# Kernel tuning notes

Hardware: AMD Instinct MI355X
Metric: run time of the kernel (lower is better)

Reference implementation:

```python
import jax, jax.numpy as jnp
import numpy as np


def setup_inputs() -> dict:
    key = jax.random.key(0)
    k0, k1, k2, k3 = jax.random.split(key, 4)
    B, S, D, F, E = 2, 2048, 1024, 4096, 8
    hidden_states = jax.random.normal(k0, (B, S, D), dtype=jnp.float32)
    Wr = jax.random.normal(k1, (E, D), dtype=jnp.float32) * 0.02   # router Linear weight [E, D]
    W1 = jax.random.normal(k2, (E, D, F), dtype=jnp.float32) * 0.02  # expert w1 (transposed torch layout)
    W2 = jax.random.normal(k3, (E, F, D), dtype=jnp.float32) * 0.02  # expert w2
    return {"hidden_states": hidden_states, "Wr": Wr, "W1": W1, "W2": W2, "top_k": 2}


def reference(hidden_states, Wr, W1, W2, top_k):
    # hidden_states: [B, S, D]; Wr: [E, D]; W1: [E, D, F]; W2: [E, F, D]
    E = Wr.shape[0]
    dt = hidden_states.dtype

    # Router: logits -> top-k expert indices. NOTE: the original module computes
    # softmax routing weights over the top-k logits but never applies them in the
    # combine step, so the output is an UNWEIGHTED sum over selected experts.
    router_logits = jnp.einsum('bsd,ed->bse', hidden_states, Wr)
    _, topk_idx = jax.lax.top_k(router_logits, top_k)            # [B, S, K]

    # mask[b,s,e] = 1 if expert e is in token (b,s)'s top-k (indices are distinct)
    mask = (jax.nn.one_hot(topk_idx, E, dtype=dt).sum(axis=-2) > 0).astype(dt)  # [B, S, E]

    # Dense per-expert FFN (SiLU MLP, no bias, dropout=identity in eval):
    h = jax.nn.silu(jnp.einsum('bsd,edf->bsef', hidden_states, W1))  # [B, S, E, F]
    y = jnp.einsum('bsef,efd->bsed', h, W2)                          # [B, S, E, D]

    # Combine: unweighted sum over selected experts (faithful to source)
    return jnp.einsum('bsed,bse->bsd', y, mask)
```

## Files before the change

kernel.cpp:

```cpp
#include <hip/hip_runtime.h>
#include <hip/hip_bf16.h>
#include <stdint.h>

#define TOKENS 4096
#define DDIM 1024
#define FDIM 4096
#define NEXP 8
#define BM 128
#define BN 128
#define BK2 32

typedef __attribute__((ext_vector_type(4))) float f32x4;
typedef __attribute__((ext_vector_type(8))) short short8;

__device__ __forceinline__ unsigned short f2bf(float f) {
    union { float f; uint32_t u; } v; v.f = f;
    uint32_t u = v.u;
    return (unsigned short)((u + 0x7fff + ((u >> 16) & 1)) >> 16);
}

#define BARRIER() asm volatile("s_barrier" ::: "memory")
#define WAIT_VM0() asm volatile("s_waitcnt vmcnt(0)" ::: "memory")
#define WAIT_VM4() asm volatile("s_waitcnt vmcnt(4)" ::: "memory")
#define WAIT_VM8() asm volatile("s_waitcnt vmcnt(8)" ::: "memory")
#define WAIT_LGKM0() asm volatile("s_waitcnt lgkmcnt(0)" ::: "memory")
#define GLDS(SRC, DST) __builtin_amdgcn_global_load_lds( \
    (const __attribute__((address_space(1))) void*)(SRC), \
    (__attribute__((address_space(3))) void*)(DST), 16, 0, 0)

__device__ __forceinline__ short8 dsr(uint32_t addr) {
    short8 d;
    asm volatile("ds_read_b128 %0, %1" : "=v"(d) : "v"(addr));
    return d;
}

__global__ __launch_bounds__(256) void cvt_x(const float* __restrict__ x,
                                             unsigned short* __restrict__ xb, int n) {
    int i = (blockIdx.x * 256 + threadIdx.x) * 8;
    if (i >= n) return;
    float4 a = *(const float4*)(x + i);
    float4 b = *(const float4*)(x + i + 4);
    short8 o;
    o[0] = f2bf(a.x); o[1] = f2bf(a.y); o[2] = f2bf(a.z); o[3] = f2bf(a.w);
    o[4] = f2bf(b.x); o[5] = f2bf(b.y); o[6] = f2bf(b.z); o[7] = f2bf(b.w);
    *(short8*)(xb + i) = o;
}

__global__ __launch_bounds__(256) void transpose_cvt(const float* __restrict__ in,
                                                     unsigned short* __restrict__ out,
                                                     int R, int C) {
    __shared__ float tile[32][33];
    int e = blockIdx.z;
    int r0 = blockIdx.y * 32, c0 = blockIdx.x * 32;
    const float* src = in + (size_t)e * R * C;
    unsigned short* dst = out + (size_t)e * R * C;
    int t = threadIdx.x;
    int rr = t >> 3;
    int cc = (t & 7) * 4;
    float4 v = *(const float4*)(src + (size_t)(r0 + rr) * C + c0 + cc);
    tile[rr][cc + 0] = v.x; tile[rr][cc + 1] = v.y;
    tile[rr][cc + 2] = v.z; tile[rr][cc + 3] = v.w;
    __syncthreads();
    int oc = rr;
    int orr = cc;
    ushort4 o;
    o.x = f2bf(tile[orr + 0][oc]);
    o.y = f2bf(tile[orr + 1][oc]);
    o.z = f2bf(tile[orr + 2][oc]);
    o.w = f2bf(tile[orr + 3][oc]);
    *(ushort4*)(dst + (size_t)(c0 + oc) * R + r0 + orr) = o;
}

__global__ __launch_bounds__(256) void router(const float* __restrict__ x,
                                              const float* __restrict__ wr,
                                              int* __restrict__ cnt,
                                              int* __restrict__ list) {
    __shared__ float wl[NEXP * DDIM];
    int t = threadIdx.x;
    for (int i = t; i < NEXP * DDIM; i += 256) wl[i] = wr[i];
    __syncthreads();
    int tok = blockIdx.x * 4 + (t >> 6);
    int lane = t & 63;
    float acc[NEXP];
#pragma unroll
    for (int e = 0; e < NEXP; e++) acc[e] = 0.f;
    const float* xr = x + (size_t)tok * DDIM;
    for (int d = lane; d < DDIM; d += 64) {
        float xv = xr[d];
#pragma unroll
        for (int e = 0; e < NEXP; e++) acc[e] += xv * wl[e * DDIM + d];
    }
#pragma unroll
    for (int e = 0; e < NEXP; e++) {
#pragma unroll
        for (int off = 32; off; off >>= 1) acc[e] += __shfl_xor(acc[e], off);
    }
    if (lane == 0) {
        int e1 = 0; float v1 = acc[0];
        for (int e = 1; e < NEXP; e++) if (acc[e] > v1) { v1 = acc[e]; e1 = e; }
        int e2 = -1; float v2 = -1e30f;
        for (int e = 0; e < NEXP; e++) if (e != e1 && acc[e] > v2) { v2 = acc[e]; e2 = e; }
        int p1 = atomicAdd(&cnt[e1], 1);
        list[e1 * TOKENS + p1] = tok;
        int p2 = atomicAdd(&cnt[e2], 1);
        list[e2 * TOKENS + p2] = tok;
    }
}

__global__ void setup(const int* __restrict__ cnt, int* __restrict__ off,
                      int* __restrict__ wbA, int* __restrict__ wbB,
                      int* __restrict__ qctr, int* __restrict__ tot) {
    if (threadIdx.x == 0) {
        int s = 0, ta = 0, tb = 0;
        for (int e = 0; e < NEXP; e++) {
            off[e] = s; s += cnt[e];
            wbA[e] = ta; wbB[e] = tb;
            int nt = (cnt[e] + BM - 1) / BM;
            ta += nt * (FDIM / BN);
            tb += nt * (DDIM / BN);
        }
        wbA[NEXP] = ta; wbB[NEXP] = tb;
        tot[0] = ta; tot[1] = tb;
        qctr[0] = 0; qctr[1] = 0;
    }
}

template <bool GATHER_A, bool SILU>
__global__ __launch_bounds__(256, 2) void gemm_moe5(
    const unsigned short* __restrict__ Abase,
    const unsigned short* __restrict__ Wt,
    const int* __restrict__ cnt, const int* __restrict__ off,
    const int* __restrict__ list,
    const int* __restrict__ wbase,
    int* __restrict__ qctr, const int* __restrict__ tot,
    unsigned short* __restrict__ Hout,
    float* __restrict__ Yout,
    int KD, int NDIM) {
    __shared__ alignas(16) unsigned short As[4][BM * BK2];
    __shared__ alignas(16) unsigned short Bs[4][BN * BK2];
    __shared__ int wsh;

    int t = threadIdx.x;
    int lane = t & 63;
    int wid = t >> 6;
    int wm = wid >> 1, wn = wid & 1;
    int r16 = lane & 15, g = lane >> 4;
    const int total = *tot;

    uint32_t asBase = (uint32_t)(uintptr_t)&As[0][0];
    uint32_t bsBase = (uint32_t)(uintptr_t)&Bs[0][0];
    uint32_t aAdr[4], bAdr[4];
#pragma unroll
    for (int mi = 0; mi < 4; mi++) {
        int row = wm * 64 + mi * 16 + r16;
        aAdr[mi] = asBase + row * 64 + ((g ^ ((row >> 1) & 3)) << 4);
    }
#pragma unroll
    for (int nj = 0; nj < 4; nj++) {
        int row = wn * 64 + nj * 16 + r16;
        bAdr[nj] = bsBase + row * 64 + ((g ^ ((row >> 1) & 3)) << 4);
    }

    for (;;) {
        if (t == 0) wsh = atomicAdd(qctr, 1);
        __syncthreads();
        int w = wsh;
        if (w >= total) break;

        int e = 0;
        while (e < NEXP - 1 && w >= wbase[e + 1]) e++;
        w -= wbase[e];
        int n_e = cnt[e];
        int ntm = (n_e + BM - 1) >> 7;
        int by = w / ntm;
        int mtile = w - by * ntm;
        int m0 = mtile * BM;
        int n0 = by * BN;
        int base = off[e];

        const unsigned short* pA[2];
        const unsigned short* pB[2];
        int ldsOff[2];
#pragma unroll
        for (int i = 0; i < 2; i++) {
            int c = i * 256 + t;
            int row = c >> 2, p = c & 3;
            int cg = p ^ ((row >> 1) & 3);
            int arow = m0 + row; if (arow >= n_e) arow = n_e - 1;
            size_t grow = GATHER_A ? (size_t)list[e * TOKENS + arow] : (size_t)(base + arow);
            pA[i] = Abase + grow * (size_t)KD + (cg << 3);
            pB[i] = Wt + ((size_t)e * NDIM + n0 + row) * (size_t)KD + (cg << 3);
            ldsOff[i] = c * 16;
        }

        f32x4 acc[4][4];
#pragma unroll
        for (int i = 0; i < 4; i++)
#pragma unroll
            for (int j = 0; j < 4; j++) acc[i][j] = f32x4{0.f, 0.f, 0.f, 0.f};

#pragma unroll
        for (int s = 0; s < 3; ++s) {
#pragma unroll
            for (int i = 0; i < 2; i++) { GLDS(pA[i], (char*)As[s] + ldsOff[i]); pA[i] += BK2; }
#pragma unroll
            for (int i = 0; i < 2; i++) { GLDS(pB[i], (char*)Bs[s] + ldsOff[i]); pB[i] += BK2; }
        }
        WAIT_VM8();
        BARRIER();

        const int NT = KD / BK2;
        for (int tk = 0; tk < NT; ++tk) {
            const uint32_t sb = (uint32_t)(tk & 3) << 13;

            if (tk + 3 < NT) {
                const int ws_ = (tk + 3) & 3;
#pragma unroll
                for (int i = 0; i < 2; i++) { GLDS(pA[i], (char*)As[ws_] + ldsOff[i]); pA[i] += BK2; }
#pragma unroll
                for (int i = 0; i < 2; i++) { GLDS(pB[i], (char*)Bs[ws_] + ldsOff[i]); pB[i] += BK2; }
            }

            short8 a0 = dsr(aAdr[0] + sb);
            short8 a1 = dsr(aAdr[1] + sb);
            short8 a2 = dsr(aAdr[2] + sb);
            short8 a3 = dsr(aAdr[3] + sb);
            short8 b0 = dsr(bAdr[0] + sb);
            short8 b1 = dsr(bAdr[1] + sb);
            short8 b2 = dsr(bAdr[2] + sb);
            short8 b3 = dsr(bAdr[3] + sb);
            WAIT_LGKM0();
            __builtin_amdgcn_sched_barrier(0);

            __builtin_amdgcn_s_setprio(1);
            acc[0][0] = __builtin_amdgcn_mfma_f32_16x16x32_bf16(a0, b0, acc[0][0], 0, 0, 0);
            acc[0][1] = __builtin_amdgcn_mfma_f32_16x16x32_bf16(a0, b1, acc[0][1], 0, 0, 0);
            acc[0][2] = __builtin_amdgcn_mfma_f32_16x16x32_bf16(a0, b2, acc[0][2], 0, 0, 0);
            acc[0][3] = __builtin_amdgcn_mfma_f32_16x16x32_bf16(a0, b3, acc[0][3], 0, 0, 0);
            acc[1][0] = __builtin_amdgcn_mfma_f32_16x16x32_bf16(a1, b0, acc[1][0], 0, 0, 0);
            acc[1][1] = __builtin_amdgcn_mfma_f32_16x16x32_bf16(a1, b1, acc[1][1], 0, 0, 0);
            acc[1][2] = __builtin_amdgcn_mfma_f32_16x16x32_bf16(a1, b2, acc[1][2], 0, 0, 0);
            acc[1][3] = __builtin_amdgcn_mfma_f32_16x16x32_bf16(a1, b3, acc[1][3], 0, 0, 0);
            acc[2][0] = __builtin_amdgcn_mfma_f32_16x16x32_bf16(a2, b0, acc[2][0], 0, 0, 0);
            acc[2][1] = __builtin_amdgcn_mfma_f32_16x16x32_bf16(a2, b1, acc[2][1], 0, 0, 0);
            acc[2][2] = __builtin_amdgcn_mfma_f32_16x16x32_bf16(a2, b2, acc[2][2], 0, 0, 0);
            acc[2][3] = __builtin_amdgcn_mfma_f32_16x16x32_bf16(a2, b3, acc[2][3], 0, 0, 0);
            acc[3][0] = __builtin_amdgcn_mfma_f32_16x16x32_bf16(a3, b0, acc[3][0], 0, 0, 0);
            acc[3][1] = __builtin_amdgcn_mfma_f32_16x16x32_bf16(a3, b1, acc[3][1], 0, 0, 0);
            acc[3][2] = __builtin_amdgcn_mfma_f32_16x16x32_bf16(a3, b2, acc[3][2], 0, 0, 0);
            acc[3][3] = __builtin_amdgcn_mfma_f32_16x16x32_bf16(a3, b3, acc[3][3], 0, 0, 0);
            __builtin_amdgcn_s_setprio(0);

            if (tk + 1 < NT) {
                if (tk + 3 < NT)      WAIT_VM8();
                else if (tk + 2 < NT) WAIT_VM4();
                else                  WAIT_VM0();
                BARRIER();
            }
        }

#pragma unroll
        for (int mi = 0; mi < 4; ++mi) {
#pragma unroll
            for (int nj = 0; nj < 4; ++nj) {
#pragma unroll
                for (int qq = 0; qq < 4; ++qq) {
                    int lr = wm * 64 + mi * 16 + g * 4 + qq;
                    if (m0 + lr < n_e) {
                        int col = n0 + wn * 64 + nj * 16 + r16;
                        float v = acc[mi][nj][qq];
                        if (SILU) {
                            v = v / (1.f + __expf(-v));
                            Hout[(size_t)(base + m0 + lr) * NDIM + col] = f2bf(v);
                        } else {
                            int tok = list[e * TOKENS + m0 + lr];
                            atomicAdd(&Yout[(size_t)tok * NDIM + col], v);
                        }
                    }
                }
            }
        }
    }
}

extern "C" void kernel_launch(void* const* d_in, const int* in_sizes, int n_in,
                              void* d_out, int out_size, void* d_ws, size_t ws_size,
                              hipStream_t stream) {
    const float* X  = (const float*)d_in[0];
    const float* Wr = (const float*)d_in[1];
    const float* W1 = (const float*)d_in[2];
    const float* W2 = (const float*)d_in[3];
    float* Y = (float*)d_out;

    char* ws = (char*)d_ws;
    int* cnt  = (int*)(ws + 0);
    int* off  = (int*)(ws + 64);
    int* wbA  = (int*)(ws + 128);
    int* wbB  = (int*)(ws + 192);
    int* qctr = (int*)(ws + 256);
    int* tot  = (int*)(ws + 288);
    int* list = (int*)(ws + 1024);
    unsigned short* Xb = (unsigned short*)(ws + (1ull << 20));
    unsigned short* WT = (unsigned short*)(ws + (16ull << 20));
    unsigned short* H  = (unsigned short*)(ws + (80ull << 20));

    hipMemsetAsync(d_out, 0, (size_t)out_size * sizeof(float), stream);
    hipMemsetAsync(cnt, 0, 32, stream);

    cvt_x<<<TOKENS * DDIM / (256 * 8), 256, 0, stream>>>(X, Xb, TOKENS * DDIM);
    router<<<TOKENS / 4, 256, 0, stream>>>(X, Wr, cnt, list);
    setup<<<1, 64, 0, stream>>>(cnt, off, wbA, wbB, qctr, tot);

    transpose_cvt<<<dim3(FDIM / 32, DDIM / 32, NEXP), 256, 0, stream>>>(W1, WT, DDIM, FDIM);
    gemm_moe5<true, true><<<512, 256, 0, stream>>>(
        Xb, WT, cnt, off, list, wbA, qctr + 0, tot + 0, H, nullptr, DDIM, FDIM);

    transpose_cvt<<<dim3(DDIM / 32, FDIM / 32, NEXP), 256, 0, stream>>>(W2, WT, FDIM, DDIM);
    gemm_moe5<false, false><<<512, 256, 0, stream>>>(
        H, WT, cnt, off, list, wbB, qctr + 1, tot + 1, nullptr, Y, FDIM, DDIM);
}
```

Before: 477.0 us.

## Enlarge MoE GEMM tiles to 256-row blocks with 512 threads and split-K for second GEMM

Replaces the 128x128x32 four-stage tiled grouped GEMM with 512-thread blocks computing 256-row tiles (256 columns for the first GEMM, 128 for the second), using 64-wide K steps, double buffering and a new XOR swizzle. The second GEMM splits K in two, relying on the existing atomic-add epilogue so more tiles are available. The aim is higher arithmetic intensity and fewer redundant weight and activation loads per FLOP. The cost is a shallower pipeline that waits on all outstanding loads every step, more registers per thread, and more tile padding for experts with fewer tokens.

```diff
diff --git a/kernel.cpp b/kernel.cpp
--- a/kernel.cpp
+++ b/kernel.cpp
@@ -6,9 +6,6 @@
 #define DDIM 1024
 #define FDIM 4096
 #define NEXP 8
-#define BM 128
-#define BN 128
-#define BK2 32
 
 typedef __attribute__((ext_vector_type(4))) float f32x4;
 typedef __attribute__((ext_vector_type(8))) short short8;
@@ -21,8 +18,6 @@
 
 #define BARRIER() asm volatile("s_barrier" ::: "memory")
 #define WAIT_VM0() asm volatile("s_waitcnt vmcnt(0)" ::: "memory")
-#define WAIT_VM4() asm volatile("s_waitcnt vmcnt(4)" ::: "memory")
-#define WAIT_VM8() asm volatile("s_waitcnt vmcnt(8)" ::: "memory")
 #define WAIT_LGKM0() asm volatile("s_waitcnt lgkmcnt(0)" ::: "memory")
 #define GLDS(SRC, DST) __builtin_amdgcn_global_load_lds( \
     (const __attribute__((address_space(1))) void*)(SRC), \
@@ -109,57 +104,59 @@
 
 __global__ void setup(const int* __restrict__ cnt, int* __restrict__ off,
                       int* __restrict__ wbA, int* __restrict__ wbB,
-                      int* __restrict__ qctr, int* __restrict__ tot) {
+                      int* __restrict__ qctr) {
     if (threadIdx.x == 0) {
         int s = 0, ta = 0, tb = 0;
         for (int e = 0; e < NEXP; e++) {
             off[e] = s; s += cnt[e];
             wbA[e] = ta; wbB[e] = tb;
-            int nt = (cnt[e] + BM - 1) / BM;
-            ta += nt * (FDIM / BN);
-            tb += nt * (DDIM / BN);
+            int ntm = (cnt[e] + 255) >> 8;
+            ta += ntm * 16;
+            tb += ntm * 16;
         }
         wbA[NEXP] = ta; wbB[NEXP] = tb;
-        tot[0] = ta; tot[1] = tb;
         qctr[0] = 0; qctr[1] = 0;
     }
 }
 
-template <bool GATHER_A, bool SILU>
-__global__ __launch_bounds__(256, 2) void gemm_moe5(
+template <int BN_, bool GATHER_A, bool SILU, int KSPLIT>
+__global__ __launch_bounds__(512, 2) void gemm_moe7(
     const unsigned short* __restrict__ Abase,
     const unsigned short* __restrict__ Wt,
     const int* __restrict__ cnt, const int* __restrict__ off,
     const int* __restrict__ list,
     const int* __restrict__ wbase,
-    int* __restrict__ qctr, const int* __restrict__ tot,
+    int* __restrict__ qctr,
     unsigned short* __restrict__ Hout,
     float* __restrict__ Yout,
-    int KD, int NDIM) {
-    __shared__ alignas(16) unsigned short As[4][BM * BK2];
-    __shared__ alignas(16) unsigned short Bs[4][BN * BK2];
+    int KD, int KLEN, int NW) {
+    constexpr int NF = BN_ / 64;
+    constexpr int WCOL = BN_ / 4;
+    constexpr int NA = 4;
+    constexpr int NB = BN_ * 8 / 512;
+    constexpr uint32_t SLOTA = 256 * 64 * 2;
+    constexpr uint32_t SLOTB = BN_ * 64 * 2;
+
+    __shared__ alignas(16) unsigned short As[2][256 * 64];
+    __shared__ alignas(16) unsigned short Bs[2][BN_ * 64];
     __shared__ int wsh;
 
-    int t = threadIdx.x;
-    int lane = t & 63;
-    int wid = t >> 6;
-    int wm = wid >> 1, wn = wid & 1;
-    int r16 = lane & 15, g = lane >> 4;
-    const int total = *tot;
-
-    uint32_t asBase = (uint32_t)(uintptr_t)&As[0][0];
-    uint32_t bsBase = (uint32_t)(uintptr_t)&Bs[0][0];
-    uint32_t aAdr[4], bAdr[4];
-#pragma unroll
-    for (int mi = 0; mi < 4; mi++) {
-        int row = wm * 64 + mi * 16 + r16;
-        aAdr[mi] = asBase + row * 64 + ((g ^ ((row >> 1) & 3)) << 4);
-    }
-#pragma unroll
-    for (int nj = 0; nj < 4; nj++) {
-        int row = wn * 64 + nj * 16 + r16;
-        bAdr[nj] = bsBase + row * 64 + ((g ^ ((row >> 1) & 3)) << 4);
-    }
+    const int t = threadIdx.x;
+    const int lane = t & 63;
+    const int wid = t >> 6;
+    const int wm = wid >> 2, wn = wid & 3;
+    const int r16 = lane & 15, g = lane >> 4;
+    const int total = wbase[NEXP];
+
+    const uint32_t asB = (uint32_t)(uintptr_t)&As[0][0];
+    const uint32_t bsB = (uint32_t)(uintptr_t)&Bs[0][0];
+    const uint32_t swz = (uint32_t)(r16 & 7) << 4;
+    const uint32_t g16 = (uint32_t)g << 4;
+    uint32_t rA[8], rB[NF];
+#pragma unroll
+    for (int mi = 0; mi < 8; mi++) rA[mi] = asB + (uint32_t)(wm * 128 + mi * 16 + r16) * 128u;
+#pragma unroll
+    for (int nj = 0; nj < NF; nj++) rB[nj] = bsB + (uint32_t)(wn * WCOL + nj * 16 + r16) * 128u;
 
     for (;;) {
         if (t == 0) wsh = atomicAdd(qctr, 1);
@@ -170,111 +167,100 @@
         int e = 0;
         while (e < NEXP - 1 && w >= wbase[e + 1]) e++;
         w -= wbase[e];
-        int n_e = cnt[e];
-        int ntm = (n_e + BM - 1) >> 7;
-        int by = w / ntm;
-        int mtile = w - by * ntm;
-        int m0 = mtile * BM;
-        int n0 = by * BN;
-        int base = off[e];
-
-        const unsigned short* pA[2];
-        const unsigned short* pB[2];
-        int ldsOff[2];
-#pragma unroll
-        for (int i = 0; i < 2; i++) {
-            int c = i * 256 + t;
-            int row = c >> 2, p = c & 3;
-            int cg = p ^ ((row >> 1) & 3);
-            int arow = m0 + row; if (arow >= n_e) arow = n_e - 1;
-            size_t grow = GATHER_A ? (size_t)list[e * TOKENS + arow] : (size_t)(base + arow);
-            pA[i] = Abase + grow * (size_t)KD + (cg << 3);
-            pB[i] = Wt + ((size_t)e * NDIM + n0 + row) * (size_t)KD + (cg << 3);
-            ldsOff[i] = c * 16;
-        }
-
-        f32x4 acc[4][4];
-#pragma unroll
-        for (int i = 0; i < 4; i++)
-#pragma unroll
-            for (int j = 0; j < 4; j++) acc[i][j] = f32x4{0.f, 0.f, 0.f, 0.f};
-
-#pragma unroll
-        for (int s = 0; s < 3; ++s) {
-#pragma unroll
-            for (int i = 0; i < 2; i++) { GLDS(pA[i], (char*)As[s] + ldsOff[i]); pA[i] += BK2; }
-#pragma unroll
-            for (int i = 0; i < 2; i++) { GLDS(pB[i], (char*)Bs[s] + ldsOff[i]); pB[i] += BK2; }
-        }
-        WAIT_VM8();
+        const int n_e = cnt[e];
+        const int ntm = (n_e + 255) >> 8;
+        int idx = w / ntm;
+        const int mtile = w - idx * ntm;
+        int kc = 0;
+        if (KSPLIT == 2) { kc = idx & 1; idx >>= 1; }
+        const int m0 = mtile * 256;
+        const int n0 = idx * BN_;
+        const int base = off[e];
+        const int k0 = kc * KLEN;
+
+        const unsigned short* pA[NA];
+        const unsigned short* pB[NB];
+#pragma unroll
+        for (int i = 0; i < NA; i++) {
+            int c = i * 512 + t;
+            int row = c >> 3, p = c & 7, cg = p ^ (row & 7);
+            int arow = m0 + row; if (arow > n_e - 1) arow = n_e - 1;
+            size_t gr = GATHER_A ? (size_t)list[e * TOKENS + arow] : (size_t)(base + arow);
+            pA[i] = Abase + gr * (size_t)KD + k0 + cg * 8;
+        }
+#pragma unroll
+        for (int i = 0; i < NB; i++) {
+            int c = i * 512 + t;
+            int row = c >> 3, p = c & 7, cg = p ^ (row & 7);
+            pB[i] = Wt + ((size_t)e * NW + n0 + row) * (size_t)KD + k0 + cg * 8;
+        }
+
+        f32x4 acc[8][NF];
+#pragma unroll
+        for (int i = 0; i < 8; i++)
+#pragma unroll
+            for (int j = 0; j < NF; j++) acc[i][j] = f32x4{0.f, 0.f, 0.f, 0.f};
+
+#pragma unroll
+        for (int i = 0; i < NA; i++) { GLDS(pA[i], (char*)As[0] + t * 16 + i * 8192); pA[i] += 64; }
+#pragma unroll
+        for (int i = 0; i < NB; i++) { GLDS(pB[i], (char*)Bs[0] + t * 16 + i * 8192); pB[i] += 64; }
+        WAIT_VM0();
         BARRIER();
 
-        const int NT = KD / BK2;
+        const int NT = KLEN >> 6;
         for (int tk = 0; tk < NT; ++tk) {
-            const uint32_t sb = (uint32_t)(tk & 3) << 13;
-
-            if (tk + 3 < NT) {
-                const int ws_ = (tk + 3) & 3;
-#pragma unroll
-                for (int i = 0; i < 2; i++) { GLDS(pA[i], (char*)As[ws_] + ldsOff[i]); pA[i] += BK2; }
-#pragma unroll
-                for (int i = 0; i < 2; i++) { GLDS(pB[i], (char*)Bs[ws_] + ldsOff[i]); pB[i] += BK2; }
+            const uint32_t coA = (tk & 1) ? SLOTA : 0u;
+            const uint32_t coB = (tk & 1) ? SLOTB : 0u;
+
+            if (tk + 1 < NT) {
+                char* Ad = (char*)As[(tk & 1) ^ 1];
+                char* Bd = (char*)Bs[(tk & 1) ^ 1];
+#pragma unroll
+                for (int i = 0; i < NA; i++) { GLDS(pA[i], Ad + t * 16 + i * 8192); pA[i] += 64; }
+#pragma unroll
+                for (int i = 0; i < NB; i++) { GLDS(pB[i], Bd + t * 16 + i * 8192); pB[i] += 64; }
             }
 
-            short8 a0 = dsr(aAdr[0] + sb);
-            short8 a1 = dsr(aAdr[1] + sb);
-            short8 a2 = dsr(aAdr[2] + sb);
-            short8 a3 = dsr(aAdr[3] + sb);
-            short8 b0 = dsr(bAdr[0] + sb);
-            short8 b1 = dsr(bAdr[1] + sb);
-            short8 b2 = dsr(bAdr[2] + sb);
-            short8 b3 = dsr(bAdr[3] + sb);
-            WAIT_LGKM0();
-            __builtin_amdgcn_sched_barrier(0);
-
-            __builtin_amdgcn_s_setprio(1);
-            acc[0][0] = __builtin_amdgcn_mfma_f32_16x16x32_bf16(a0, b0, acc[0][0], 0, 0, 0);
-            acc[0][1] = __builtin_amdgcn_mfma_f32_16x16x32_bf16(a0, b1, acc[0][1], 0, 0, 0);
-            acc[0][2] = __builtin_amdgcn_mfma_f32_16x16x32_bf16(a0, b2, acc[0][2], 0, 0, 0);
-            acc[0][3] = __builtin_amdgcn_mfma_f32_16x16x32_bf16(a0, b3, acc[0][3], 0, 0, 0);
-            acc[1][0] = __builtin_amdgcn_mfma_f32_16x16x32_bf16(a1, b0, acc[1][0], 0, 0, 0);
-            acc[1][1] = __builtin_amdgcn_mfma_f32_16x16x32_bf16(a1, b1, acc[1][1], 0, 0, 0);
-            acc[1][2] = __builtin_amdgcn_mfma_f32_16x16x32_bf16(a1, b2, acc[1][2], 0, 0, 0);
-            acc[1][3] = __builtin_amdgcn_mfma_f32_16x16x32_bf16(a1, b3, acc[1][3], 0, 0, 0);
-            acc[2][0] = __builtin_amdgcn_mfma_f32_16x16x32_bf16(a2, b0, acc[2][0], 0, 0, 0);
-            acc[2][1] = __builtin_amdgcn_mfma_f32_16x16x32_bf16(a2, b1, acc[2][1], 0, 0, 0);
-            acc[2][2] = __builtin_amdgcn_mfma_f32_16x16x32_bf16(a2, b2, acc[2][2], 0, 0, 0);
-            acc[2][3] = __builtin_amdgcn_mfma_f32_16x16x32_bf16(a2, b3, acc[2][3], 0, 0, 0);
-            acc[3][0] = __builtin_amdgcn_mfma_f32_16x16x32_bf16(a3, b0, acc[3][0], 0, 0, 0);
-            acc[3][1] = __builtin_amdgcn_mfma_f32_16x16x32_bf16(a3, b1, acc[3][1], 0, 0, 0);
-            acc[3][2] = __builtin_amdgcn_mfma_f32_16x16x32_bf16(a3, b2, acc[3][2], 0, 0, 0);
-            acc[3][3] = __builtin_amdgcn_mfma_f32_16x16x32_bf16(a3, b3, acc[3][3], 0, 0, 0);
-            __builtin_amdgcn_s_setprio(0);
-
-            if (tk + 1 < NT) {
-                if (tk + 3 < NT)      WAIT_VM8();
-                else if (tk + 2 < NT) WAIT_VM4();
-                else                  WAIT_VM0();
-                BARRIER();
+#pragma unroll
+            for (int s = 0; s < 2; s++) {
+                const uint32_t cb = (((uint32_t)(s * 64) + g16) ^ swz);
+                short8 a[8], b[NF];
+#pragma unroll
+                for (int mi = 0; mi < 8; mi++) a[mi] = dsr(rA[mi] + coA + cb);
+#pragma unroll
+                for (int nj = 0; nj < NF; nj++) b[nj] = dsr(rB[nj] + coB + cb);
+                WAIT_LGKM0();
+                __builtin_amdgcn_sched_barrier(0);
+                __builtin_amdgcn_s_setprio(1);
+#pragma unroll
+                for (int mi = 0; mi < 8; mi++)
+#pragma unroll
+                    for (int nj = 0; nj < NF; nj++)
+                        acc[mi][nj] = __builtin_amdgcn_mfma_f32_16x16x32_bf16(a[mi], b[nj], acc[mi][nj], 0, 0, 0);
+                __builtin_amdgcn_s_setprio(0);
             }
-        }
-
-#pragma unroll
-        for (int mi = 0; mi < 4; ++mi) {
-#pragma unroll
-            for (int nj = 0; nj < 4; ++nj) {
+
+            WAIT_VM0();
+            BARRIER();
+        }
+
+#pragma unroll
+        for (int mi = 0; mi < 8; ++mi) {
+#pragma unroll
+            for (int nj = 0; nj < NF; ++nj) {
 #pragma unroll
                 for (int qq = 0; qq < 4; ++qq) {
-                    int lr = wm * 64 + mi * 16 + g * 4 + qq;
+                    int lr = wm * 128 + mi * 16 + g * 4 + qq;
                     if (m0 + lr < n_e) {
-                        int col = n0 + wn * 64 + nj * 16 + r16;
+                        int col = n0 + wn * WCOL + nj * 16 + r16;
                         float v = acc[mi][nj][qq];
                         if (SILU) {
                             v = v / (1.f + __expf(-v));
-                            Hout[(size_t)(base + m0 + lr) * NDIM + col] = f2bf(v);
+                            Hout[(size_t)(base + m0 + lr) * NW + col] = f2bf(v);
                         } else {
                             int tok = list[e * TOKENS + m0 + lr];
-                            atomicAdd(&Yout[(size_t)tok * NDIM + col], v);
+                            atomicAdd(&Yout[(size_t)tok * NW + col], v);
                         }
                     }
                 }
@@ -298,7 +284,6 @@
     int* wbA  = (int*)(ws + 128);
     int* wbB  = (int*)(ws + 192);
     int* qctr = (int*)(ws + 256);
-    int* tot  = (int*)(ws + 288);
     int* list = (int*)(ws + 1024);
     unsigned short* Xb = (unsigned short*)(ws + (1ull << 20));
     unsigned short* WT = (unsigned short*)(ws + (16ull << 20));
@@ -309,13 +294,13 @@
 
     cvt_x<<<TOKENS * DDIM / (256 * 8), 256, 0, stream>>>(X, Xb, TOKENS * DDIM);
     router<<<TOKENS / 4, 256, 0, stream>>>(X, Wr, cnt, list);
-    setup<<<1, 64, 0, stream>>>(cnt, off, wbA, wbB, qctr, tot);
+    setup<<<1, 64, 0, stream>>>(cnt, off, wbA, wbB, qctr);
 
     transpose_cvt<<<dim3(FDIM / 32, DDIM / 32, NEXP), 256, 0, stream>>>(W1, WT, DDIM, FDIM);
-    gemm_moe5<true, true><<<512, 256, 0, stream>>>(
-        Xb, WT, cnt, off, list, wbA, qctr + 0, tot + 0, H, nullptr, DDIM, FDIM);
+    gemm_moe7<256, true, true, 1><<<256, 512, 0, stream>>>(
+        Xb, WT, cnt, off, list, wbA, qctr + 0, H, nullptr, DDIM, DDIM, FDIM);
 
     transpose_cvt<<<dim3(DDIM / 32, FDIM / 32, NEXP), 256, 0, stream>>>(W2, WT, FDIM, DDIM);
-    gemm_moe5<false, false><<<512, 256, 0, stream>>>(
-        H, WT, cnt, off, list, wbB, qctr + 1, tot + 1, nullptr, Y, FDIM, DDIM);
-}
+    gemm_moe7<128, false, false, 2><<<256, 512, 0, stream>>>(
+        H, WT, cnt, off, list, wbB, qctr + 1, nullptr, Y, FDIM, FDIM / 2, DDIM);
+}
```

Result: slower. 492.3 us (+3.2%).

## Split-K second GEMM, triple-buffer LDS for three blocks per CU

Applied to the files above, without the earlier changes.

Splits the K dimension of the down-projection GEMM in two, giving it twice as many work tiles; the existing atomicAdd epilogue combines the partial results. Shrinks the LDS ring from four stages to three with rotating offsets, which frees shared memory so launch bounds can allow three blocks per CU, and raises the persistent grid from 512 to 768 blocks. The intent is better CU fill and latency hiding. The cost is a shallower prefetch pipeline and twice as many atomic adds on the output.

```diff
diff --git a/kernel.cpp b/kernel.cpp
--- a/kernel.cpp
+++ b/kernel.cpp
@@ -22,7 +22,6 @@
 #define BARRIER() asm volatile("s_barrier" ::: "memory")
 #define WAIT_VM0() asm volatile("s_waitcnt vmcnt(0)" ::: "memory")
 #define WAIT_VM4() asm volatile("s_waitcnt vmcnt(4)" ::: "memory")
-#define WAIT_VM8() asm volatile("s_waitcnt vmcnt(8)" ::: "memory")
 #define WAIT_LGKM0() asm volatile("s_waitcnt lgkmcnt(0)" ::: "memory")
 #define GLDS(SRC, DST) __builtin_amdgcn_global_load_lds( \
     (const __attribute__((address_space(1))) void*)(SRC), \
@@ -109,56 +108,55 @@
 
 __global__ void setup(const int* __restrict__ cnt, int* __restrict__ off,
                       int* __restrict__ wbA, int* __restrict__ wbB,
-                      int* __restrict__ qctr, int* __restrict__ tot) {
+                      int* __restrict__ qctr) {
     if (threadIdx.x == 0) {
         int s = 0, ta = 0, tb = 0;
         for (int e = 0; e < NEXP; e++) {
             off[e] = s; s += cnt[e];
             wbA[e] = ta; wbB[e] = tb;
-            int nt = (cnt[e] + BM - 1) / BM;
-            ta += nt * (FDIM / BN);
-            tb += nt * (DDIM / BN);
+            int ntm = (cnt[e] + BM - 1) / BM;
+            ta += ntm * (FDIM / BN);
+            tb += ntm * (DDIM / BN) * 2;
         }
         wbA[NEXP] = ta; wbB[NEXP] = tb;
-        tot[0] = ta; tot[1] = tb;
         qctr[0] = 0; qctr[1] = 0;
     }
 }
 
-template <bool GATHER_A, bool SILU>
-__global__ __launch_bounds__(256, 2) void gemm_moe5(
+template <bool GATHER_A, bool SILU, int KSPLIT>
+__global__ __launch_bounds__(256, 3) void gemm_moe8(
     const unsigned short* __restrict__ Abase,
     const unsigned short* __restrict__ Wt,
     const int* __restrict__ cnt, const int* __restrict__ off,
     const int* __restrict__ list,
     const int* __restrict__ wbase,
-    int* __restrict__ qctr, const int* __restrict__ tot,
+    int* __restrict__ qctr,
     unsigned short* __restrict__ Hout,
     float* __restrict__ Yout,
-    int KD, int NDIM) {
-    __shared__ alignas(16) unsigned short As[4][BM * BK2];
-    __shared__ alignas(16) unsigned short Bs[4][BN * BK2];
+    int KD, int KLEN, int NW) {
+    __shared__ alignas(16) unsigned short As[3][BM * BK2];
+    __shared__ alignas(16) unsigned short Bs[3][BN * BK2];
     __shared__ int wsh;
 
-    int t = threadIdx.x;
-    int lane = t & 63;
-    int wid = t >> 6;
-    int wm = wid >> 1, wn = wid & 1;
-    int r16 = lane & 15, g = lane >> 4;
-    const int total = *tot;
-
-    uint32_t asBase = (uint32_t)(uintptr_t)&As[0][0];
-    uint32_t bsBase = (uint32_t)(uintptr_t)&Bs[0][0];
+    const int t = threadIdx.x;
+    const int lane = t & 63;
+    const int wid = t >> 6;
+    const int wm = wid >> 1, wn = wid & 1;
+    const int r16 = lane & 15, g = lane >> 4;
+    const int total = wbase[NEXP];
+
+    const uint32_t asB = (uint32_t)(uintptr_t)&As[0][0];
+    const uint32_t bsB = (uint32_t)(uintptr_t)&Bs[0][0];
     uint32_t aAdr[4], bAdr[4];
 #pragma unroll
     for (int mi = 0; mi < 4; mi++) {
         int row = wm * 64 + mi * 16 + r16;
-        aAdr[mi] = asBase + row * 64 + ((g ^ ((row >> 1) & 3)) << 4);
+        aAdr[mi] = asB + row * 64 + ((g ^ ((row >> 1) & 3)) << 4);
     }
 #pragma unroll
     for (int nj = 0; nj < 4; nj++) {
         int row = wn * 64 + nj * 16 + r16;
-        bAdr[nj] = bsBase + row * 64 + ((g ^ ((row >> 1) & 3)) << 4);
+        bAdr[nj] = bsB + row * 64 + ((g ^ ((row >> 1) & 3)) << 4);
     }
 
     for (;;) {
@@ -170,13 +168,16 @@
         int e = 0;
         while (e < NEXP - 1 && w >= wbase[e + 1]) e++;
         w -= wbase[e];
-        int n_e = cnt[e];
-        int ntm = (n_e + BM - 1) >> 7;
-        int by = w / ntm;
-        int mtile = w - by * ntm;
-        int m0 = mtile * BM;
-        int n0 = by * BN;
-        int base = off[e];
+        const int n_e = cnt[e];
+        const int ntm = (n_e + BM - 1) >> 7;
+        int idx = w / ntm;
+        const int mtile = w - idx * ntm;
+        int kc = 0;
+        if (KSPLIT == 2) { kc = idx & 1; idx >>= 1; }
+        const int m0 = mtile * BM;
+        const int n0 = idx * BN;
+        const int base = off[e];
+        const int k0 = kc * KLEN;
 
         const unsigned short* pA[2];
         const unsigned short* pB[2];
@@ -188,8 +189,8 @@
             int cg = p ^ ((row >> 1) & 3);
             int arow = m0 + row; if (arow >= n_e) arow = n_e - 1;
             size_t grow = GATHER_A ? (size_t)list[e * TOKENS + arow] : (size_t)(base + arow);
-            pA[i] = Abase + grow * (size_t)KD + (cg << 3);
-            pB[i] = Wt + ((size_t)e * NDIM + n0 + row) * (size_t)KD + (cg << 3);
+            pA[i] = Abase + grow * (size_t)KD + k0 + (cg << 3);
+            pB[i] = Wt + ((size_t)e * NW + n0 + row) * (size_t)KD + k0 + (cg << 3);
             ldsOff[i] = c * 16;
         }
 
@@ -200,35 +201,34 @@
             for (int j = 0; j < 4; j++) acc[i][j] = f32x4{0.f, 0.f, 0.f, 0.f};
 
 #pragma unroll
-        for (int s = 0; s < 3; ++s) {
+        for (int s = 0; s < 2; ++s) {
 #pragma unroll
             for (int i = 0; i < 2; i++) { GLDS(pA[i], (char*)As[s] + ldsOff[i]); pA[i] += BK2; }
 #pragma unroll
             for (int i = 0; i < 2; i++) { GLDS(pB[i], (char*)Bs[s] + ldsOff[i]); pB[i] += BK2; }
         }
-        WAIT_VM8();
+        WAIT_VM4();
         BARRIER();
 
-        const int NT = KD / BK2;
+        uint32_t o0 = 0, o1 = 8192, o2 = 16384;
+
+        const int NT = KLEN / BK2;
         for (int tk = 0; tk < NT; ++tk) {
-            const uint32_t sb = (uint32_t)(tk & 3) << 13;
-
-            if (tk + 3 < NT) {
-                const int ws_ = (tk + 3) & 3;
-#pragma unroll
-                for (int i = 0; i < 2; i++) { GLDS(pA[i], (char*)As[ws_] + ldsOff[i]); pA[i] += BK2; }
-#pragma unroll
-                for (int i = 0; i < 2; i++) { GLDS(pB[i], (char*)Bs[ws_] + ldsOff[i]); pB[i] += BK2; }
+            if (tk + 2 < NT) {
+#pragma unroll
+                for (int i = 0; i < 2; i++) { GLDS(pA[i], (char*)As[0] + o2 + ldsOff[i]); pA[i] += BK2; }
+#pragma unroll
+                for (int i = 0; i < 2; i++) { GLDS(pB[i], (char*)Bs[0] + o2 + ldsOff[i]); pB[i] += BK2; }
             }
 
-            short8 a0 = dsr(aAdr[0] + sb);
-            short8 a1 = dsr(aAdr[1] + sb);
-            short8 a2 = dsr(aAdr[2] + sb);
-            short8 a3 = dsr(aAdr[3] + sb);
-            short8 b0 = dsr(bAdr[0] + sb);
-            short8 b1 = dsr(bAdr[1] + sb);
-            short8 b2 = dsr(bAdr[2] + sb);
-            short8 b3 = dsr(bAdr[3] + sb);
+            short8 a0 = dsr(aAdr[0] + o0);
+            short8 a1 = dsr(aAdr[1] + o0);
+            short8 a2 = dsr(aAdr[2] + o0);
+            short8 a3 = dsr(aAdr[3] + o0);
+            short8 b0 = dsr(bAdr[0] + o0);
+            short8 b1 = dsr(bAdr[1] + o0);
+            short8 b2 = dsr(bAdr[2] + o0);
+            short8 b3 = dsr(bAdr[3] + o0);
             WAIT_LGKM0();
             __builtin_amdgcn_sched_barrier(0);
 
@@ -252,11 +252,11 @@
             __builtin_amdgcn_s_setprio(0);
 
             if (tk + 1 < NT) {
-                if (tk + 3 < NT)      WAIT_VM8();
-                else if (tk + 2 < NT) WAIT_VM4();
-                else                  WAIT_VM0();
+                if (tk + 2 < NT) WAIT_VM4();
+                else             WAIT_VM0();
                 BARRIER();
             }
+            uint32_t tmp = o0; o0 = o1; o1 = o2; o2 = tmp;
         }
 
 #pragma unroll
@@ -271,10 +271,10 @@
                         float v = acc[mi][nj][qq];
                         if (SILU) {
                             v = v / (1.f + __expf(-v));
-                            Hout[(size_t)(base + m0 + lr) * NDIM + col] = f2bf(v);
+                            Hout[(size_t)(base + m0 + lr) * NW + col] = f2bf(v);
                         } else {
                             int tok = list[e * TOKENS + m0 + lr];
-                            atomicAdd(&Yout[(size_t)tok * NDIM + col], v);
+                            atomicAdd(&Yout[(size_t)tok * NW + col], v);
                         }
                     }
                 }
@@ -298,7 +298,6 @@
     int* wbA  = (int*)(ws + 128);
     int* wbB  = (int*)(ws + 192);
     int* qctr = (int*)(ws + 256);
-    int* tot  = (int*)(ws + 288);
     int* list = (int*)(ws + 1024);
     unsigned short* Xb = (unsigned short*)(ws + (1ull << 20));
     unsigned short* WT = (unsigned short*)(ws + (16ull << 20));
@@ -309,13 +308,13 @@
 
     cvt_x<<<TOKENS * DDIM / (256 * 8), 256, 0, stream>>>(X, Xb, TOKENS * DDIM);
     router<<<TOKENS / 4, 256, 0, stream>>>(X, Wr, cnt, list);
-    setup<<<1, 64, 0, stream>>>(cnt, off, wbA, wbB, qctr, tot);
+    setup<<<1, 64, 0, stream>>>(cnt, off, wbA, wbB, qctr);
 
     transpose_cvt<<<dim3(FDIM / 32, DDIM / 32, NEXP), 256, 0, stream>>>(W1, WT, DDIM, FDIM);
-    gemm_moe5<true, true><<<512, 256, 0, stream>>>(
-        Xb, WT, cnt, off, list, wbA, qctr + 0, tot + 0, H, nullptr, DDIM, FDIM);
+    gemm_moe8<true, true, 1><<<768, 256, 0, stream>>>(
+        Xb, WT, cnt, off, list, wbA, qctr + 0, H, nullptr, DDIM, DDIM, FDIM);
 
     transpose_cvt<<<dim3(DDIM / 32, FDIM / 32, NEXP), 256, 0, stream>>>(W2, WT, FDIM, DDIM);
-    gemm_moe5<false, false><<<512, 256, 0, stream>>>(
-        H, WT, cnt, off, list, wbB, qctr + 1, tot + 1, nullptr, Y, FDIM, DDIM);
-}
+    gemm_moe8<false, false, 2><<<768, 256, 0, stream>>>(
+        H, WT, cnt, off, list, wbB, qctr + 1, nullptr, Y, FDIM, FDIM / 2, DDIM);
+}
```

Result: faster. 463.1 us (-2.9%).
